# Kernel optimization log

Measured on AMD Instinct MI355X. Metric: run time of the kernel, lower is better.

The kernel has to match this reference:

```python
import jax, jax.numpy as jnp
import numpy as np

B = 4096          # fused tokens (batch)
E = 1024          # attnConfig embed_size == MoE emb_size
OUT = E // 4      # per-branch feature dim (self.output)
N_EXP = 8         # number of experts
TOP = 2           # top-k routing
H = 8             # attention heads
HD = E // H       # head dim
HID = 4 * E       # expert MLP hidden
IMG = 64 * 64     # flattened single-channel image
W_IMP = 0.01      # importance loss weight


def setup_inputs() -> dict:
    key = jax.random.key(0)
    ks = jax.random.split(key, 24)
    n = lambda i, shp, sc=1.0: jax.random.normal(ks[i], shp, jnp.float32) * sc
    inp = {
        'source': n(0, (B, 1, 64, 64)),
        'target': n(1, (B, 1, 64, 64)),
        'background': n(2, (B, 1, 64, 64)),
        'image': n(3, (B, E)),
        'text': n(4, (B, E)),
        # shared encoder (stub: flatten -> fc to OUT, shared across s/t/b)
        'W_enc': n(5, (IMG, OUT), 0.02), 'b_enc': jnp.zeros((OUT,), jnp.float32),
        # linerImg
        'W_img': n(6, (E, OUT), 0.02), 'b_img': jnp.zeros((OUT,), jnp.float32),
        # cross attention
        'Wq': n(7, (E, E), 0.02), 'bq': jnp.zeros((E,), jnp.float32),
        'Wk': n(8, (E, E), 0.02), 'bk': jnp.zeros((E,), jnp.float32),
        'Wv': n(9, (E, E), 0.02), 'bv': jnp.zeros((E,), jnp.float32),
        'Wo': n(10, (E, E), 0.02), 'bo': jnp.zeros((E,), jnp.float32),
        # gate
        'W_gate': n(11, (E, N_EXP), 0.02), 'b_gate': jnp.zeros((N_EXP,), jnp.float32),
        # experts: per-expert 2-layer MLP E->HID->E
        'W1': n(12, (N_EXP, E, HID), 0.02), 'b1': jnp.zeros((N_EXP, HID), jnp.float32),
        'W2': n(13, (N_EXP, HID, E), 0.02), 'b2': jnp.zeros((N_EXP, E), jnp.float32),
    }
    return inp


def reference(source, target, background, image, text,
              W_enc, b_enc, W_img, b_img,
              Wq, bq, Wk, bk, Wv, bv, Wo, bo,
              W_gate, b_gate, W1, b1, W2, b2):
    enc = lambda a: a.reshape(a.shape[0], -1) @ W_enc + b_enc      # shared_encoder stub
    s = enc(source); t = enc(target); bg = enc(background)        # [B, OUT] each
    img = jax.nn.silu(image @ W_img + b_img)                      # [B, OUT]
    x = jnp.concatenate([s, t, bg, img], axis=1)                  # [B, E] visionFeatures

    # cross attention with seq_len 1 for both x (query) and text (key/value)
    q = (x @ Wq + bq).reshape(B, H, HD)
    k = (text @ Wk + bk).reshape(B, H, HD)
    v = (text @ Wv + bv).reshape(B, H, HD)
    scores = jnp.sum(q * k, axis=-1, keepdims=True) / jnp.sqrt(jnp.float32(HD))  # [B,H,1]
    attw = jax.nn.softmax(scores[..., None], axis=-1)[..., 0]     # softmax over 1 key == 1
    att = (attw * v).reshape(B, E) @ Wo + bo                       # [B, E]

    gate_logits = att @ W_gate + b_gate                            # [B, N_EXP]
    gate_prob = jax.nn.softmax(gate_logits, axis=-1)               # eval mode: no noise
    top_w, top_idx = jax.lax.top_k(gate_prob, TOP)                 # [B, TOP]
    top_w = jax.nn.softmax(top_w, axis=-1)                         # renormalize over top-k

    # dense-dispatch equivalent of the per-expert gather/index_add loop
    h = jax.nn.gelu(jnp.einsum('be,neh->nbh', x, W1) + b1[:, None, :])   # [N,B,HID]
    y_all = jnp.einsum('nbh,nhe->nbe', h, W2) + b2[:, None, :]           # [N,B,E]
    combine = jnp.zeros((B, N_EXP), jnp.float32).at[
        jnp.arange(B)[:, None], top_idx].add(top_w)                      # [B,N]
    y = jnp.einsum('nbe,bn->be', y_all, combine)                          # [B,E]

    importance = gate_prob.sum(axis=0)                             # [N_EXP]
    importance_loss = W_IMP * (jnp.std(importance, ddof=1) / jnp.mean(importance)) ** 2
    return (y, gate_prob, importance_loss)
```

## Files before the change

### kernel.cpp

```cpp
#include <hip/hip_runtime.h>
#include <hip/hip_bf16.h>
#include <stdint.h>

typedef __bf16 bf16_t;
typedef bf16_t bf16x8 __attribute__((ext_vector_type(8)));
typedef float f32x4 __attribute__((ext_vector_type(4)));
typedef uint16_t u16x8 __attribute__((ext_vector_type(8)));

static constexpr int B_TOK  = 4096;
static constexpr int E_DIM  = 1024;
static constexpr int N_EXPC = 8;
static constexpr int HID    = 4096;
static constexpr int IMGSZ  = 4096;
static constexpr int NSLOT  = 2 * B_TOK;
static constexpr int NTIL   = 71;

#define DEVI __device__ __forceinline__

DEVI int imin(int a, int b) { return a < b ? a : b; }

DEVI uint16_t f2bf(float f) {
  union { float f; uint32_t u; } v; v.f = f;
  uint32_t u = v.u;
  return (uint16_t)((u + 0x7FFFu + ((u >> 16) & 1u)) >> 16);
}

DEVI float bf2f(uint16_t u) {
  union { uint32_t i; float f; } v; v.i = (uint32_t)u << 16; return v.f;
}

DEVI void gload_lds16(const void* g, void* l) {
  __builtin_amdgcn_global_load_lds((const __attribute__((address_space(1))) void*)g,
                                   (__attribute__((address_space(3))) void*)l, 16, 0, 0);
}

template<int N> DEVI void waitv() {
  if constexpr (N == 0)       asm volatile("s_waitcnt vmcnt(0)" ::: "memory");
  else if constexpr (N == 4)  asm volatile("s_waitcnt vmcnt(4)" ::: "memory");
  else if constexpr (N == 8)  asm volatile("s_waitcnt vmcnt(8)" ::: "memory");
  else if constexpr (N == 10) asm volatile("s_waitcnt vmcnt(10)" ::: "memory");
}

#define BAR() do { __builtin_amdgcn_sched_barrier(0); __builtin_amdgcn_s_barrier(); \
                   __builtin_amdgcn_sched_barrier(0); } while (0)

#define MFMA16(a, b, c) __builtin_amdgcn_mfma_f32_16x16x32_bf16((a), (b), (c), 0, 0, 0)

DEVI void transW_body(int bid, const float* W1, const float* W2,
                      const float* We, const float* Wi,
                      uint16_t* W1T, uint16_t* W2T, uint16_t* WeT, uint16_t* WiT,
                      float (*tile)[65])
{
  const float* in; uint16_t* out; int R, C, c0, r0;
  if (bid < 8192) {
    int e = bid >> 10, rem = bid & 1023;
    R = 1024; C = 4096;
    c0 = (rem & 63) * 64; r0 = (rem >> 6) * 64;
    in = W1 + (size_t)e * R * C; out = W1T + (size_t)e * R * C;
  } else if (bid < 16384) {
    int i = bid - 8192; int e = i >> 10, rem = i & 1023;
    R = 4096; C = 1024;
    c0 = (rem & 15) * 64; r0 = (rem >> 4) * 64;
    in = W2 + (size_t)e * R * C; out = W2T + (size_t)e * R * C;
  } else if (bid < 16640) {
    int i = bid - 16384;
    R = 4096; C = 256;
    c0 = (i & 3) * 64; r0 = (i >> 2) * 64;
    in = We; out = WeT;
  } else {
    int i = bid - 16640;
    R = 1024; C = 256;
    c0 = (i & 3) * 64; r0 = (i >> 2) * 64;
    in = Wi; out = WiT;
  }
  int t = threadIdx.x;
  #pragma unroll
  for (int i = 0; i < 4; ++i) {
    int rr = i * 16 + (t >> 4), c4 = (t & 15) * 4;
    f32x4 v = *(const f32x4*)&in[(size_t)(r0 + rr) * C + c0 + c4];
    tile[rr][c4 + 0] = v[0]; tile[rr][c4 + 1] = v[1];
    tile[rr][c4 + 2] = v[2]; tile[rr][c4 + 3] = v[3];
  }
  __syncthreads();
  #pragma unroll
  for (int i = 0; i < 2; ++i) {
    int c = i * 32 + (t >> 3), j = t & 7;
    u16x8 o;
    #pragma unroll
    for (int k = 0; k < 8; ++k) o[k] = f2bf(tile[j * 8 + k][c]);
    *(u16x8*)&out[(size_t)(c0 + c) * R + r0 + j * 8] = o;
  }
}

DEVI void matf_body(int kblk, const float* W, const float* G, float* out)
{
  int k = kblk * 4 + (threadIdx.x >> 6);
  int lane = threadIdx.x & 63;
  float a0 = 0.f, a1 = 0.f, a2 = 0.f, a3 = 0.f, a4 = 0.f, a5 = 0.f, a6 = 0.f, a7 = 0.f;
  for (int m = lane; m < E_DIM; m += 64) {
    float w = W[(size_t)k * E_DIM + m];
    const float* gm = &G[m * 8];
    a0 = __builtin_fmaf(w, gm[0], a0); a1 = __builtin_fmaf(w, gm[1], a1);
    a2 = __builtin_fmaf(w, gm[2], a2); a3 = __builtin_fmaf(w, gm[3], a3);
    a4 = __builtin_fmaf(w, gm[4], a4); a5 = __builtin_fmaf(w, gm[5], a5);
    a6 = __builtin_fmaf(w, gm[6], a6); a7 = __builtin_fmaf(w, gm[7], a7);
  }
  #pragma unroll
  for (int off = 32; off; off >>= 1) {
    a0 += __shfl_xor(a0, off); a1 += __shfl_xor(a1, off);
    a2 += __shfl_xor(a2, off); a3 += __shfl_xor(a3, off);
    a4 += __shfl_xor(a4, off); a5 += __shfl_xor(a5, off);
    a6 += __shfl_xor(a6, off); a7 += __shfl_xor(a7, off);
  }
  if (lane == 0) {
    float* o = &out[k * 8];
    o[0] = a0; o[1] = a1; o[2] = a2; o[3] = a3;
    o[4] = a4; o[5] = a5; o[6] = a6; o[7] = a7;
  }
}

__global__ __launch_bounds__(256)
void prep1_k(const float* __restrict__ W1, const float* __restrict__ W2,
             const float* __restrict__ We, const float* __restrict__ Wi,
             uint16_t* __restrict__ W1T, uint16_t* __restrict__ W2T,
             uint16_t* __restrict__ WeT, uint16_t* __restrict__ WiT,
             const float* __restrict__ Wo, const float* __restrict__ Wg,
             float* __restrict__ g1c,
             const float* __restrict__ bv, float* __restrict__ part,
             int* __restrict__ counts)
{
  __shared__ float tile[64][65];
  int bid = blockIdx.x;
  if (bid < 16704) {
    transW_body(bid, W1, W2, We, Wi, W1T, W2T, WeT, WiT, tile);
  } else if (bid < 16960) {
    matf_body(bid - 16704, Wo, Wg, g1c);
  } else if (bid < 16968) {
    int b = bid - 16960, t = threadIdx.x;
    f32x4 acc = {0.f, 0.f, 0.f, 0.f};
    for (int k = b * 128; k < b * 128 + 128; ++k) {
      float s = bv[k];
      f32x4 w = *(const f32x4*)&Wo[(size_t)k * E_DIM + t * 4];
      acc[0] = __builtin_fmaf(s, w[0], acc[0]);
      acc[1] = __builtin_fmaf(s, w[1], acc[1]);
      acc[2] = __builtin_fmaf(s, w[2], acc[2]);
      acc[3] = __builtin_fmaf(s, w[3], acc[3]);
    }
    *(f32x4*)&part[(size_t)b * E_DIM + t * 4] = acc;
  } else {
    if (threadIdx.x < 8) counts[threadIdx.x] = 0;
  }
}

__global__ __launch_bounds__(256)
void prep2_k(const float* __restrict__ Wv, const float* __restrict__ g1c,
             float* __restrict__ G3,
             const float* __restrict__ part, const float* __restrict__ bo,
             const float* __restrict__ Wg, const float* __restrict__ bg,
             float* __restrict__ gb)
{
  int bid = blockIdx.x;
  if (bid < 256) {
    matf_body(bid, Wv, g1c, G3);
  } else {
    __shared__ float t1s[E_DIM];
    int t = threadIdx.x;
    for (int j = t; j < E_DIM; j += 256) {
      float s = bo[j];
      #pragma unroll
      for (int b = 0; b < 8; ++b) s += part[(size_t)b * E_DIM + j];
      t1s[j] = s;
    }
    __syncthreads();
    int wave = t >> 6, lane = t & 63;
    #pragma unroll
    for (int ei = 0; ei < 2; ++ei) {
      int e = wave * 2 + ei;
      float s = 0.f;
      for (int m = lane; m < E_DIM; m += 64) s = __builtin_fmaf(t1s[m], Wg[m * 8 + e], s);
      #pragma unroll
      for (int off = 32; off; off >>= 1) s += __shfl_xor(s, off);
      if (lane == 0) gb[e] = s + bg[e];
    }
  }
}

__global__ __launch_bounds__(256, 3)
void encgate_k(const float* __restrict__ F0, const float* __restrict__ F1,
               const float* __restrict__ F2, const float* __restrict__ Fimg,
               const uint16_t* __restrict__ BTe, const uint16_t* __restrict__ BTi,
               float* __restrict__ Penc, float* __restrict__ Pimg,
               const float* __restrict__ text, const float* __restrict__ G3,
               const float* __restrict__ gb, float* __restrict__ gate_out,
               int* __restrict__ topIdx, float* __restrict__ topW,
               int* __restrict__ counts)
{
  __shared__ __align__(16) char shbuf[3 * 8192];
  int bid = blockIdx.x;
  int t = threadIdx.x;

  if (bid >= 896) {
    int b = bid - 896;
    float* sT = (float*)shbuf;
    float* lg = (float*)(shbuf + E_DIM * 4);
    *(f32x4*)&sT[t * 4] = *(const f32x4*)&text[(size_t)b * E_DIM + t * 4];
    __syncthreads();
    int wave = t >> 6, lane = t & 63;
    #pragma unroll
    for (int ei = 0; ei < 2; ++ei) {
      int e = wave * 2 + ei;
      float s = 0.f;
      for (int k = lane; k < E_DIM; k += 64) s = __builtin_fmaf(sT[k], G3[k * 8 + e], s);
      #pragma unroll
      for (int off = 32; off; off >>= 1) s += __shfl_down(s, off);
      if (lane == 0) lg[e] = s + gb[e];
    }
    __syncthreads();
    if (t == 0) {
      float p[8];
      float mx = lg[0];
      for (int i = 1; i < 8; i++) mx = fmaxf(mx, lg[i]);
      float den = 0.f;
      for (int i = 0; i < 8; i++) { p[i] = __expf(lg[i] - mx); den += p[i]; }
      float inv = 1.f / den;
      for (int i = 0; i < 8; i++) { p[i] *= inv; gate_out[(size_t)b * 8 + i] = p[i]; }
      int i1 = 0;
      for (int i = 1; i < 8; i++) if (p[i] > p[i1]) i1 = i;
      int i2 = (i1 == 0) ? 1 : 0;
      for (int i = 0; i < 8; i++) if (i != i1 && p[i] > p[i2]) i2 = i;
      float ex = __expf(p[i2] - p[i1]);
      float w1 = 1.f / (1.f + ex), w2 = ex / (1.f + ex);
      topIdx[b * 2] = i1; topIdx[b * 2 + 1] = i2;
      topW[b * 2] = w1;  topW[b * 2 + 1] = w2;
      atomicAdd(&counts[i1], 1);
      atomicAdd(&counts[i2], 1);
    }
    return;
  }

  int z = bid >> 7, yb = (bid >> 6) & 1, xb = bid & 63;
  const float* Af; const uint16_t* BT; float* P; int K, Kc, k0;
  if (z < 6) {
    int br = z >> 1, kc = z & 1;
    Af = (br == 0) ? F0 : (br == 1) ? F1 : F2;
    BT = BTe; P = Penc + (size_t)z * B_TOK * 256;
    K = IMGSZ; Kc = IMGSZ / 2; k0 = kc * Kc;
  } else {
    Af = Fimg; BT = BTi; P = Pimg;
    K = E_DIM; Kc = E_DIM; k0 = 0;
  }
  int rowBase = xb * 64, nt = yb;

  char* sB = shbuf;
  int wave = t >> 6, lane = t & 63;
  int fr = lane & 15, q4 = lane >> 4;

  const float* gA = Af + (size_t)(rowBase + wave * 16 + fr) * K + k0 + q4 * 8;

  int rloc = t >> 2;
  int ssw = ((t & 3) ^ (rloc & 3)) * 8;
  const uint16_t* gB0 = BT + (size_t)(nt * 128 + rloc) * K + k0 + ssw;
  const uint16_t* gB1 = gB0 + (size_t)64 * K;

  auto STB = [&](int kt, int c) {
    gload_lds16(gB0 + kt * 32, sB + c * 8192 + wave * 1024);
    gload_lds16(gB1 + kt * 32, sB + c * 8192 + 4096 + wave * 1024);
  };

  f32x4 acc[8];
  #pragma unroll
  for (int n = 0; n < 8; ++n) acc[n] = f32x4{0.f, 0.f, 0.f, 0.f};

  int nk = Kc >> 5;
  STB(0, 0); STB(1, 1);
  f32x4 aE0 = *(const f32x4*)(gA),      aE1 = *(const f32x4*)(gA + 4);
  f32x4 aO0 = *(const f32x4*)(gA + 32), aO1 = *(const f32x4*)(gA + 36);
  int c0 = 0, c2 = 2;
  int bRow = (q4 ^ (fr & 3)) * 16;

  auto step = [&](int kt, f32x4& aX0, f32x4& aX1) {
    bool m2 = kt + 2 < nk;
    if (m2) STB(kt + 2, c2);
    bf16x8 a;
    a[0] = (bf16_t)aX0[0]; a[1] = (bf16_t)aX0[1]; a[2] = (bf16_t)aX0[2]; a[3] = (bf16_t)aX0[3];
    a[4] = (bf16_t)aX1[0]; a[5] = (bf16_t)aX1[1]; a[6] = (bf16_t)aX1[2]; a[7] = (bf16_t)aX1[3];
    int kp = m2 ? kt + 2 : kt;
    aX0 = *(const f32x4*)(gA + kp * 32);
    aX1 = *(const f32x4*)(gA + kp * 32 + 4);
    if (m2) waitv<10>(); else waitv<0>();
    BAR();
    const char* bb = sB + c0 * 8192;
    bf16x8 bfr[8];
    #pragma unroll
    for (int n = 0; n < 8; ++n)
      bfr[n] = *(const bf16x8*)(bb + n * 1024 + fr * 64 + bRow);
    #pragma unroll
    for (int n = 0; n < 8; ++n) acc[n] = MFMA16(a, bfr[n], acc[n]);
    BAR();
    c0 = (c0 == 2) ? 0 : c0 + 1;
    c2 = (c2 == 2) ? 0 : c2 + 1;
  };

  for (int kt = 0; kt < nk; kt += 2) {
    step(kt, aE0, aE1);
    step(kt + 1, aO0, aO1);
  }

  #pragma unroll
  for (int n = 0; n < 8; ++n) {
    int col = nt * 128 + n * 16 + fr;
    #pragma unroll
    for (int r = 0; r < 4; ++r) {
      int row = rowBase + wave * 16 + q4 * 4 + r;
      P[(size_t)row * 256 + col] = acc[n][r];
    }
  }
}

template<int BN, int EPI, bool GATHER, int NT>
__global__ __launch_bounds__(256, 3)
void gemm_p(const uint16_t* __restrict__ Ab, int lda,
            const uint16_t* __restrict__ BT, void* __restrict__ Cv, int ldc,
            const float* __restrict__ bias, int K,
            const int* __restrict__ meta, const int* __restrict__ perm,
            size_t bStride, int biasStride)
{
  constexpr int HN = BN / 2, FN = BN / 32;
  constexpr int OPS = (BN == 128 ? 4 : 3);
  constexpr int TOTAL = NTIL * NT, Q = TOTAL / 8, FULLB = 64 * NT;
  int bid = blockIdx.x;
  int wg = (bid & 7) * Q + (bid >> 3);
  int mtile, nt;
  if (wg < FULLB) { int rem = wg % (8 * NT); mtile = (wg / (8 * NT)) * 8 + (rem & 7); nt = rem >> 3; }
  else            { int rem = wg - FULLB;    mtile = 64 + rem % 7;                    nt = rem / 7; }
  if (mtile >= meta[0]) return;
  int e = meta[1 + 3 * mtile], rowBase = meta[2 + 3 * mtile], rows = meta[3 + 3 * mtile];
  const uint16_t* Bt = BT + (size_t)e * bStride;
  const float* bi = bias + (size_t)e * (size_t)biasStride;

  constexpr int ABUF = 8192;
  constexpr int BBUF = (BN == 128) ? 8192 : 4096;
  __shared__ __align__(16) char sAraw[3 * ABUF];
  __shared__ __align__(16) char sBraw[3 * BBUF];

  int t = threadIdx.x, wave = t >> 6, lane = t & 63;
  int wr = wave >> 1, wc = wave & 1;

  int rB = t >> 2;
  int slB = ((t & 3) ^ (rB & 3)) * 8;
  const uint16_t* gB0 = Bt + (size_t)(nt * BN + rB) * K + slB;
  const uint16_t* gB1 = Bt + (size_t)(nt * BN + rB + 64) * K + slB;

  int r0 = t >> 2, r1 = r0 + 64;
  int sl = ((t & 3) ^ (r0 & 3)) * 8;
  int rr0 = imin(r0, rows - 1), rr1 = imin(r1, rows - 1);
  int car0 = GATHER ? perm[rowBase + rr0] : rowBase + rr0;
  int car1 = GATHER ? perm[rowBase + rr1] : rowBase + rr1;
  const uint16_t* gA0 = Ab + (size_t)car0 * lda + sl;
  const uint16_t* gA1 = Ab + (size_t)car1 * lda + sl;

  char* laW = sAraw + wave * 1024;
  char* lbW = sBraw + wave * 1024;
  auto STAGE = [&](int kt, int c) {
    int ko = kt << 5;
    char* la = laW + c * ABUF;
    char* lb = lbW + c * BBUF;
    gload_lds16(gA0 + ko, la);
    gload_lds16(gA1 + ko, la + 4096);
    gload_lds16(gB0 + ko, lb);
    if constexpr (BN == 128) gload_lds16(gB1 + ko, lb + 4096);
  };

  f32x4 acc[4][FN];
  #pragma unroll
  for (int m = 0; m < 4; m++)
    #pragma unroll
    for (int n = 0; n < FN; n++)
      acc[m][n] = f32x4{0.f, 0.f, 0.f, 0.f};

  STAGE(0, 0);
  STAGE(1, 1);

  int fr = lane & 15;
  int rdoff = ((lane >> 4) ^ (lane & 3)) * 16;
  int c0 = 0, c2 = 2;
  int nk = K >> 5;

  for (int kt = 0; kt < nk; ++kt) {
    if (kt + 2 < nk) { STAGE(kt + 2, c2); waitv<2 * OPS>(); }
    else if (kt + 1 < nk) waitv<OPS>();
    else waitv<0>();
    BAR();

    const char* bA = sAraw + c0 * ABUF;
    const char* bB = sBraw + c0 * BBUF;
    bf16x8 af[4], bfr[FN];
    #pragma unroll
    for (int m = 0; m < 4; m++)
      af[m] = *(const bf16x8*)(bA + (wr * 64 + m * 16 + fr) * 64 + rdoff);
    #pragma unroll
    for (int n = 0; n < FN; n++)
      bfr[n] = *(const bf16x8*)(bB + (wc * HN + n * 16 + fr) * 64 + rdoff);
    #pragma unroll
    for (int m = 0; m < 4; m++)
      #pragma unroll
      for (int n = 0; n < FN; n++)
        acc[m][n] = MFMA16(af[m], bfr[n], acc[m][n]);

    BAR();
    c0 = (c0 == 2) ? 0 : c0 + 1;
    c2 = (c2 == 2) ? 0 : c2 + 1;
  }

  #pragma unroll
  for (int m = 0; m < 4; m++) {
    int lrow = wr * 64 + m * 16 + (lane >> 4) * 4;
    #pragma unroll
    for (int n = 0; n < FN; n++) {
      int col = nt * BN + wc * HN + n * 16 + (lane & 15);
      float bval = bi[col];
      #pragma unroll
      for (int r = 0; r < 4; r++) {
        int lr = lrow + r;
        if (lr >= rows) continue;
        float v = acc[m][n][r] + bval;
        size_t cr = (size_t)(rowBase + lr) * ldc + col;
        if (EPI == 3) {
          float u = v + 0.044715f * v * v * v;
          v = v / (1.f + __expf(-1.5957691216057308f * u));
          ((uint16_t*)Cv)[cr] = f2bf(v);
        } else {
          ((uint16_t*)Cv)[cr] = f2bf(v);
        }
      }
    }
  }
}

__global__ __launch_bounds__(256)
void redupost_k(const float* __restrict__ Penc, const float* __restrict__ Pimg,
                const float* __restrict__ bEnc, const float* __restrict__ bImg,
                uint16_t* __restrict__ xb,
                const float* __restrict__ gate_out, float* __restrict__ out_loss,
                const int* __restrict__ counts, const int* __restrict__ topIdx,
                const float* __restrict__ topW,
                int* __restrict__ meta, int* __restrict__ perm,
                int* __restrict__ slotOf)
{
  int y = blockIdx.y, t = threadIdx.x;
  if (y < 4) {
    int row = blockIdx.x * 4 + (t >> 6);
    int c4 = (t & 63) * 4;
    bool img = (y == 3);
    const float* bias = img ? bImg : bEnc;
    f32x4 s = *(const f32x4*)&bias[c4];
    if (img) {
      s += *(const f32x4*)&Pimg[(size_t)row * 256 + c4];
      #pragma unroll
      for (int j = 0; j < 4; ++j) s[j] = s[j] / (1.f + __expf(-s[j]));
    } else {
      const float* p = Penc + (size_t)y * 2 * B_TOK * 256 + (size_t)row * 256 + c4;
      s += *(const f32x4*)p;
      s += *(const f32x4*)(p + (size_t)B_TOK * 256);
    }
    ushort4 o;
    o.x = f2bf(s[0]); o.y = f2bf(s[1]); o.z = f2bf(s[2]); o.w = f2bf(s[3]);
    *(ushort4*)&xb[(size_t)row * E_DIM + y * 256 + c4] = o;
    return;
  }
  if (blockIdx.x == 0) {
    float s[8] = {0.f, 0.f, 0.f, 0.f, 0.f, 0.f, 0.f, 0.f};
    for (int b = t; b < B_TOK; b += 256) {
      const float* g = &gate_out[(size_t)b * 8];
      #pragma unroll
      for (int e = 0; e < 8; ++e) s[e] += g[e];
    }
    __shared__ float red[8][256];
    #pragma unroll
    for (int e = 0; e < 8; ++e) red[e][t] = s[e];
    __syncthreads();
    for (int off = 128; off; off >>= 1) {
      if (t < off)
        #pragma unroll
        for (int e = 0; e < 8; ++e) red[e][t] += red[e][t + off];
      __syncthreads();
    }
    if (t == 0) {
      float m = 0.f;
      for (int e = 0; e < 8; e++) m += red[e][0];
      m *= 0.125f;
      float v = 0.f;
      for (int e = 0; e < 8; e++) { float d = red[e][0] - m; v += d * d; }
      v /= 7.f;
      out_loss[0] = 0.01f * v / (m * m);
    }
  } else if (blockIdx.x == 1) {
    __shared__ int sBases[8];
    __shared__ int sCursor[8];
    if (t == 0) {
      int a = 0, nt = 0;
      for (int e = 0; e < 8; e++) {
        sBases[e] = a; sCursor[e] = 0;
        int c = counts[e];
        for (int j = 0; j < c; j += 128) {
          meta[1 + 3 * nt] = e;
          meta[2 + 3 * nt] = a + j;
          meta[3 + 3 * nt] = (c - j < 128) ? (c - j) : 128;
          nt++;
        }
        a += c;
      }
      meta[0] = nt;
    }
    __syncthreads();
    for (int b = t; b < B_TOK; b += 256) {
      #pragma unroll
      for (int j = 0; j < 2; j++) {
        int e = topIdx[b * 2 + j];
        int pos = atomicAdd(&sCursor[e], 1);
        int slot = sBases[e] + pos;
        perm[slot] = b;
        slotOf[b * 2 + j] = slot;
      }
    }
  }
}

__global__ __launch_bounds__(256)
void combine_k(const uint16_t* __restrict__ Yg, const int* __restrict__ slotOf,
               const float* __restrict__ topW, float* __restrict__ y)
{
  int b = blockIdx.x, t = threadIdx.x;
  int s0 = slotOf[b * 2], s1 = slotOf[b * 2 + 1];
  float w0 = topW[b * 2], w1 = topW[b * 2 + 1];
  ushort4 ua = *(const ushort4*)&Yg[(size_t)s0 * E_DIM + t * 4];
  ushort4 uc = *(const ushort4*)&Yg[(size_t)s1 * E_DIM + t * 4];
  f32x4 r;
  r[0] = bf2f(ua.x) * w0 + bf2f(uc.x) * w1;
  r[1] = bf2f(ua.y) * w0 + bf2f(uc.y) * w1;
  r[2] = bf2f(ua.z) * w0 + bf2f(uc.z) * w1;
  r[3] = bf2f(ua.w) * w0 + bf2f(uc.w) * w1;
  *(f32x4*)&y[(size_t)b * E_DIM + t * 4] = r;
}

extern "C" void kernel_launch(void* const* d_in, const int* in_sizes, int n_in,
                              void* d_out, int out_size, void* d_ws, size_t ws_size,
                              hipStream_t stream)
{
  (void)in_sizes; (void)n_in; (void)out_size;
  const float* src   = (const float*)d_in[0];
  const float* tgt   = (const float*)d_in[1];
  const float* bgr   = (const float*)d_in[2];
  const float* image = (const float*)d_in[3];
  const float* text  = (const float*)d_in[4];
  const float* W_enc = (const float*)d_in[5];
  const float* b_enc = (const float*)d_in[6];
  const float* W_img = (const float*)d_in[7];
  const float* b_img = (const float*)d_in[8];
  const float* Wv    = (const float*)d_in[13];
  const float* bv    = (const float*)d_in[14];
  const float* Wo    = (const float*)d_in[15];
  const float* bo    = (const float*)d_in[16];
  const float* Wg    = (const float*)d_in[17];
  const float* bgg   = (const float*)d_in[18];
  const float* W1    = (const float*)d_in[19];
  const float* b1    = (const float*)d_in[20];
  const float* W2    = (const float*)d_in[21];
  const float* b2    = (const float*)d_in[22];

  float* out_y    = (float*)d_out;
  float* out_gate = out_y + (size_t)B_TOK * E_DIM;
  float* out_loss = out_gate + (size_t)B_TOK * N_EXPC;

  char* p = (char*)d_ws;
  auto alloc = [&](size_t bytes) { char* r = p; p += (bytes + 255) & ~(size_t)255; return r; };
  uint16_t* WencT = (uint16_t*)alloc((size_t)256 * IMGSZ * 2);
  uint16_t* WimgT = (uint16_t*)alloc((size_t)256 * E_DIM * 2);
  uint16_t* W1T   = (uint16_t*)alloc((size_t)N_EXPC * HID * E_DIM * 2);
  uint16_t* W2T   = (uint16_t*)alloc((size_t)N_EXPC * E_DIM * HID * 2);
  float* part  = (float*)alloc((size_t)8 * E_DIM * 4);
  float* g1c   = (float*)alloc((size_t)E_DIM * 8 * 4);
  float* G3    = (float*)alloc((size_t)E_DIM * 8 * 4);
  float* gbv   = (float*)alloc(64 * 4);
  int*   topIdx = (int*)alloc(B_TOK * 2 * 4);
  float* topW   = (float*)alloc(B_TOK * 2 * 4);
  int*   slotOf = (int*)alloc(B_TOK * 2 * 4);
  int*   counts = (int*)alloc(64 * 4);
  int*   meta   = (int*)alloc((1 + 3 * (NTIL + 1)) * 4 + 64);
  int*   perm   = (int*)alloc(NSLOT * 4);
  uint16_t* xbf  = (uint16_t*)alloc((size_t)B_TOK * E_DIM * 2);
  uint16_t* Hbuf = (uint16_t*)alloc((size_t)NSLOT * HID * 2);
  char* uni = alloc((size_t)7 * B_TOK * 256 * 4);
  float* Penc = (float*)uni;
  float* Pimg = Penc + (size_t)6 * B_TOK * 256;
  uint16_t* Yg = (uint16_t*)uni;
  if ((size_t)(p - (char*)d_ws) > ws_size) return;

  prep1_k<<<dim3(16969), 256, 0, stream>>>(W1, W2, W_enc, W_img, W1T, W2T, WencT, WimgT,
                                           Wo, Wg, g1c, bv, part, counts);
  prep2_k<<<dim3(257), 256, 0, stream>>>(Wv, g1c, G3, part, bo, Wg, bgg, gbv);
  encgate_k<<<dim3(896 + B_TOK), 256, 0, stream>>>(
      src, tgt, bgr, image, WencT, WimgT, Penc, Pimg,
      text, G3, gbv, out_gate, topIdx, topW, counts);
  redupost_k<<<dim3(B_TOK / 4, 5), 256, 0, stream>>>(
      Penc, Pimg, b_enc, b_img, xbf,
      out_gate, out_loss, counts, topIdx, topW, meta, perm, slotOf);

  gemm_p<128, 3, true, HID / 128><<<dim3(NTIL * (HID / 128)), 256, 0, stream>>>(
      xbf, E_DIM, W1T, Hbuf, HID, b1, E_DIM, meta, perm, (size_t)HID * E_DIM, HID);
  gemm_p<128, 1, false, E_DIM / 128><<<dim3(NTIL * (E_DIM / 128)), 256, 0, stream>>>(
      Hbuf, HID, W2T, Yg, E_DIM, b2, HID, meta, perm, (size_t)E_DIM * HID, E_DIM);

  combine_k<<<B_TOK, 256, 0, stream>>>(Yg, slotOf, topW, out_y);
}
```

Measured before the change: 583.6 us.

## Replace LDS-staged B tiles with direct register prefetch in encoder GEMM

The encoder/gate kernel stops staging B tiles through LDS with async global-to-LDS loads and barriers. Each wave now loads its own A and B fragments straight from global memory into registers, with a 4-deep software prefetch ring, and the occupancy hint is dropped from launch_bounds. This removes LDS traffic and the two barriers per k-step. In exchange, the 4 waves each fetch the same B rows redundantly, with less coalesced 16-byte loads, and register pressure rises sharply (about 4x8 bf16x8 plus A buffers), which can lower occupancy.

```diff
diff --git a/kernel.cpp b/kernel.cpp
--- a/kernel.cpp
+++ b/kernel.cpp
@@ -185,7 +185,7 @@
   }
 }
 
-__global__ __launch_bounds__(256, 3)
+__global__ __launch_bounds__(256)
 void encgate_k(const float* __restrict__ F0, const float* __restrict__ F1,
                const float* __restrict__ F2, const float* __restrict__ Fimg,
                const uint16_t* __restrict__ BTe, const uint16_t* __restrict__ BTi,
@@ -195,14 +195,13 @@
                int* __restrict__ topIdx, float* __restrict__ topW,
                int* __restrict__ counts)
 {
-  __shared__ __align__(16) char shbuf[3 * 8192];
+  __shared__ __align__(16) float sT[E_DIM];
+  __shared__ float lg[8];
   int bid = blockIdx.x;
   int t = threadIdx.x;
 
   if (bid >= 896) {
     int b = bid - 896;
-    float* sT = (float*)shbuf;
-    float* lg = (float*)(shbuf + E_DIM * 4);
     *(f32x4*)&sT[t * 4] = *(const f32x4*)&text[(size_t)b * E_DIM + t * 4];
     __syncthreads();
     int wave = t >> 6, lane = t & 63;
@@ -251,59 +250,47 @@
   }
   int rowBase = xb * 64, nt = yb;
 
-  char* sB = shbuf;
   int wave = t >> 6, lane = t & 63;
   int fr = lane & 15, q4 = lane >> 4;
 
   const float* gA = Af + (size_t)(rowBase + wave * 16 + fr) * K + k0 + q4 * 8;
-
-  int rloc = t >> 2;
-  int ssw = ((t & 3) ^ (rloc & 3)) * 8;
-  const uint16_t* gB0 = BT + (size_t)(nt * 128 + rloc) * K + k0 + ssw;
-  const uint16_t* gB1 = gB0 + (size_t)64 * K;
-
-  auto STB = [&](int kt, int c) {
-    gload_lds16(gB0 + kt * 32, sB + c * 8192 + wave * 1024);
-    gload_lds16(gB1 + kt * 32, sB + c * 8192 + 4096 + wave * 1024);
+  const uint16_t* gB[8];
+  #pragma unroll
+  for (int n = 0; n < 8; ++n)
+    gB[n] = BT + (size_t)(nt * 128 + n * 16 + fr) * K + k0 + q4 * 8;
+
+  f32x4 acc[8];
+  #pragma unroll
+  for (int n = 0; n < 8; ++n) acc[n] = f32x4{0.f, 0.f, 0.f, 0.f};
+
+  int nk = Kc >> 5;
+
+  f32x4 pa[4][2];
+  bf16x8 pb[4][8];
+  auto LOADSET = [&](int s, int kt) {
+    int ko = imin(kt, nk - 1) << 5;
+    pa[s][0] = *(const f32x4*)(gA + ko);
+    pa[s][1] = *(const f32x4*)(gA + ko + 4);
+    #pragma unroll
+    for (int n = 0; n < 8; ++n) pb[s][n] = *(const bf16x8*)(gB[n] + ko);
   };
-
-  f32x4 acc[8];
-  #pragma unroll
-  for (int n = 0; n < 8; ++n) acc[n] = f32x4{0.f, 0.f, 0.f, 0.f};
-
-  int nk = Kc >> 5;
-  STB(0, 0); STB(1, 1);
-  f32x4 aE0 = *(const f32x4*)(gA),      aE1 = *(const f32x4*)(gA + 4);
-  f32x4 aO0 = *(const f32x4*)(gA + 32), aO1 = *(const f32x4*)(gA + 36);
-  int c0 = 0, c2 = 2;
-  int bRow = (q4 ^ (fr & 3)) * 16;
-
-  auto step = [&](int kt, f32x4& aX0, f32x4& aX1) {
-    bool m2 = kt + 2 < nk;
-    if (m2) STB(kt + 2, c2);
+  auto COMP = [&](int s) {
     bf16x8 a;
-    a[0] = (bf16_t)aX0[0]; a[1] = (bf16_t)aX0[1]; a[2] = (bf16_t)aX0[2]; a[3] = (bf16_t)aX0[3];
-    a[4] = (bf16_t)aX1[0]; a[5] = (bf16_t)aX1[1]; a[6] = (bf16_t)aX1[2]; a[7] = (bf16_t)aX1[3];
-    int kp = m2 ? kt + 2 : kt;
-    aX0 = *(const f32x4*)(gA + kp * 32);
-    aX1 = *(const f32x4*)(gA + kp * 32 + 4);
-    if (m2) waitv<10>(); else waitv<0>();
-    BAR();
-    const char* bb = sB + c0 * 8192;
-    bf16x8 bfr[8];
-    #pragma unroll
-    for (int n = 0; n < 8; ++n)
-      bfr[n] = *(const bf16x8*)(bb + n * 1024 + fr * 64 + bRow);
-    #pragma unroll
-    for (int n = 0; n < 8; ++n) acc[n] = MFMA16(a, bfr[n], acc[n]);
-    BAR();
-    c0 = (c0 == 2) ? 0 : c0 + 1;
-    c2 = (c2 == 2) ? 0 : c2 + 1;
+    a[0] = (bf16_t)pa[s][0][0]; a[1] = (bf16_t)pa[s][0][1];
+    a[2] = (bf16_t)pa[s][0][2]; a[3] = (bf16_t)pa[s][0][3];
+    a[4] = (bf16_t)pa[s][1][0]; a[5] = (bf16_t)pa[s][1][1];
+    a[6] = (bf16_t)pa[s][1][2]; a[7] = (bf16_t)pa[s][1][3];
+    #pragma unroll
+    for (int n = 0; n < 8; ++n) acc[n] = MFMA16(a, pb[s][n], acc[n]);
   };
 
-  for (int kt = 0; kt < nk; kt += 2) {
-    step(kt, aE0, aE1);
-    step(kt + 1, aO0, aO1);
+  LOADSET(0, 0); LOADSET(1, 1); LOADSET(2, 2); LOADSET(3, 3);
+  for (int kt = 0; kt < nk; kt += 4) {
+    bool more = kt + 4 < nk;
+    COMP(0); if (more) LOADSET(0, kt + 4);
+    COMP(1); if (more) LOADSET(1, kt + 5);
+    COMP(2); if (more) LOADSET(2, kt + 6);
+    COMP(3); if (more) LOADSET(3, kt + 7);
   }
 
   #pragma unroll
```

New measurement: 720.1 us. 1.23x slower.

## Restructure encoder GEMM to 64-wide K tiles with double-buffered LDS staging

Applied to the files above, without the earlier changes.

The encoder/image-projection GEMM now stages B in 64-deep K tiles instead of 32, using two 16KB LDS buffers with an 8-way XOR swizzle in place of three 8KB buffers. Each barrier pair now covers two MFMA k-steps, halving barrier and wait overhead per unit of work and allowing larger loads in flight. A-operand fp32 prefetch is widened to match. The cost is more LDS per block (32KB vs 24KB), which may limit occupancy, and less pipeline depth with only two stages.

```diff
diff --git a/kernel.cpp b/kernel.cpp
--- a/kernel.cpp
+++ b/kernel.cpp
@@ -195,7 +195,7 @@
                int* __restrict__ topIdx, float* __restrict__ topW,
                int* __restrict__ counts)
 {
-  __shared__ __align__(16) char shbuf[3 * 8192];
+  __shared__ __align__(16) char shbuf[2 * 16384];
   int bid = blockIdx.x;
   int t = threadIdx.x;
 
@@ -255,55 +255,69 @@
   int wave = t >> 6, lane = t & 63;
   int fr = lane & 15, q4 = lane >> 4;
 
-  const float* gA = Af + (size_t)(rowBase + wave * 16 + fr) * K + k0 + q4 * 8;
-
-  int rloc = t >> 2;
-  int ssw = ((t & 3) ^ (rloc & 3)) * 8;
-  const uint16_t* gB0 = BT + (size_t)(nt * 128 + rloc) * K + k0 + ssw;
-  const uint16_t* gB1 = gB0 + (size_t)64 * K;
-
-  auto STB = [&](int kt, int c) {
-    gload_lds16(gB0 + kt * 32, sB + c * 8192 + wave * 1024);
-    gload_lds16(gB1 + kt * 32, sB + c * 8192 + 4096 + wave * 1024);
+  const float* gA = Af + (size_t)(rowBase + wave * 16 + fr) * K + k0;
+
+  int r8 = t >> 3;
+  int sg = ((t & 7) ^ (r8 & 7)) * 8;
+  const uint16_t* gBp0 = BT + (size_t)(nt * 128 +  0 + r8) * K + k0 + sg;
+  const uint16_t* gBp1 = BT + (size_t)(nt * 128 + 32 + r8) * K + k0 + sg;
+  const uint16_t* gBp2 = BT + (size_t)(nt * 128 + 64 + r8) * K + k0 + sg;
+  const uint16_t* gBp3 = BT + (size_t)(nt * 128 + 96 + r8) * K + k0 + sg;
+
+  auto STAGE = [&](int kt, int c) {
+    char* base = sB + c * 16384 + wave * 1024;
+    gload_lds16(gBp0 + kt * 64, base);
+    gload_lds16(gBp1 + kt * 64, base + 4096);
+    gload_lds16(gBp2 + kt * 64, base + 8192);
+    gload_lds16(gBp3 + kt * 64, base + 12288);
   };
 
   f32x4 acc[8];
   #pragma unroll
   for (int n = 0; n < 8; ++n) acc[n] = f32x4{0.f, 0.f, 0.f, 0.f};
 
-  int nk = Kc >> 5;
-  STB(0, 0); STB(1, 1);
-  f32x4 aE0 = *(const f32x4*)(gA),      aE1 = *(const f32x4*)(gA + 4);
-  f32x4 aO0 = *(const f32x4*)(gA + 32), aO1 = *(const f32x4*)(gA + 36);
-  int c0 = 0, c2 = 2;
-  int bRow = (q4 ^ (fr & 3)) * 16;
-
-  auto step = [&](int kt, f32x4& aX0, f32x4& aX1) {
+  int nk = Kc >> 6;
+
+  f32x4 paE[4], paO[4];
+  auto LA = [&](f32x4* pa, int kt) {
+    int ko = (kt << 6) + q4 * 8;
+    pa[0] = *(const f32x4*)(gA + ko);
+    pa[1] = *(const f32x4*)(gA + ko + 4);
+    pa[2] = *(const f32x4*)(gA + ko + 32);
+    pa[3] = *(const f32x4*)(gA + ko + 36);
+  };
+  auto COMP = [&](const f32x4* pa, int c) {
+    const char* bb = sB + c * 16384;
+    #pragma unroll
+    for (int ks = 0; ks < 2; ++ks) {
+      bf16x8 a;
+      a[0] = (bf16_t)pa[ks * 2][0]; a[1] = (bf16_t)pa[ks * 2][1];
+      a[2] = (bf16_t)pa[ks * 2][2]; a[3] = (bf16_t)pa[ks * 2][3];
+      a[4] = (bf16_t)pa[ks * 2 + 1][0]; a[5] = (bf16_t)pa[ks * 2 + 1][1];
+      a[6] = (bf16_t)pa[ks * 2 + 1][2]; a[7] = (bf16_t)pa[ks * 2 + 1][3];
+      int sidx = (ks * 4 + q4) ^ (fr & 7);
+      #pragma unroll
+      for (int n = 0; n < 8; ++n) {
+        bf16x8 b = *(const bf16x8*)(bb + (n * 16 + fr) * 128 + sidx * 16);
+        acc[n] = MFMA16(a, b, acc[n]);
+      }
+    }
+  };
+
+  STAGE(0, 0);
+  LA(paE, 0);
+  for (int kt = 0; kt < nk; kt += 2) {
+    STAGE(kt + 1, 1); LA(paO, kt + 1);
+    waitv<8>();
+    BAR();
+    COMP(paE, 0);
+    BAR();
     bool m2 = kt + 2 < nk;
-    if (m2) STB(kt + 2, c2);
-    bf16x8 a;
-    a[0] = (bf16_t)aX0[0]; a[1] = (bf16_t)aX0[1]; a[2] = (bf16_t)aX0[2]; a[3] = (bf16_t)aX0[3];
-    a[4] = (bf16_t)aX1[0]; a[5] = (bf16_t)aX1[1]; a[6] = (bf16_t)aX1[2]; a[7] = (bf16_t)aX1[3];
-    int kp = m2 ? kt + 2 : kt;
-    aX0 = *(const f32x4*)(gA + kp * 32);
-    aX1 = *(const f32x4*)(gA + kp * 32 + 4);
-    if (m2) waitv<10>(); else waitv<0>();
+    if (m2) { STAGE(kt + 2, 0); LA(paE, kt + 2); waitv<8>(); }
+    else waitv<0>();
     BAR();
-    const char* bb = sB + c0 * 8192;
-    bf16x8 bfr[8];
-    #pragma unroll
-    for (int n = 0; n < 8; ++n)
-      bfr[n] = *(const bf16x8*)(bb + n * 1024 + fr * 64 + bRow);
-    #pragma unroll
-    for (int n = 0; n < 8; ++n) acc[n] = MFMA16(a, bfr[n], acc[n]);
+    COMP(paO, 1);
     BAR();
-    c0 = (c0 == 2) ? 0 : c0 + 1;
-    c2 = (c2 == 2) ? 0 : c2 + 1;
-  };
-
-  for (int kt = 0; kt < nk; kt += 2) {
-    step(kt, aE0, aE1);
-    step(kt + 1, aO0, aO1);
   }
 
   #pragma unroll
```

New measurement: 571.9 us. 2.0% less time.
